# Kernel tuning notes

Measured on AMD Instinct MI355X. Metric: run time of the kernel, lower is better.

Reference implementation:

```python
import jax, jax.numpy as jnp
import numpy as np

NUM_EMBEDDINGS = 1024
EMBEDDING_DIM = 64
COMMITMENT_COST = 0.25


def setup_inputs() -> dict:
    key = jax.random.key(0)
    k1, k2 = jax.random.split(key)
    inputs = jax.random.normal(k1, (2, 64, 32, 32, 32), dtype=jnp.float32)
    embedding = jax.random.normal(k2, (NUM_EMBEDDINGS, EMBEDDING_DIM), dtype=jnp.float32)
    return {"inputs": inputs, "embedding": embedding}


def reference(inputs, embedding):
    # inputs: [B, C, D, H, W], embedding: [K, C]
    B, C, D, H, W = inputs.shape
    # flatten_permutation = [0, 2, 3, 4, 1] -> [B*D*H*W, C]
    flat_input = jnp.transpose(inputs, (0, 2, 3, 4, 1)).reshape(-1, C)
    # squared euclidean distances [N, K]
    distances = (
        jnp.sum(flat_input**2, axis=1, keepdims=True)
        + jnp.sum(embedding**2, axis=1)[None, :]
        - 2.0 * flat_input @ embedding.T
    )
    # torch.max(-distances, dim=1)[1] == argmin of distances
    encoding_indices = jnp.argmax(-distances, axis=1)  # [N]
    encoding_indices_view = encoding_indices.reshape(B, D, H, W)
    # embed: lookup then quantization_permutation [0, 4, 1, 2, 3] -> channel-first
    quantized = embedding[encoding_indices_view]            # [B, D, H, W, C]
    quantized = jnp.transpose(quantized, (0, 4, 1, 2, 3))   # [B, C, D, H, W]
    # commitment loss: MSE(stop_grad(quantized), inputs)
    loss = COMMITMENT_COST * jnp.mean((jax.lax.stop_gradient(quantized) - inputs) ** 2)
    # straight-through estimator
    quantized_st = inputs + jax.lax.stop_gradient(quantized - inputs)
    # eval path: encodings_sum = zeros(256) (hardcoded in original forward)
    encodings_sum = jnp.zeros(256, dtype=jnp.float32)
    return quantized_st, loss, encoding_indices_view, encodings_sum, embedding
```

## Files before the change

### kernel.cpp

```cpp
#include <hip/hip_runtime.h>
#include <stdint.h>

#define KCODES  1024
#define CDIM    64
#define SPATIAL 32768
#define NPOS    65536
#define NEL     4194304

#define OUT_Q    0
#define OUT_LOSS 4194304
#define OUT_IDX  4194305
#define OUT_SUM  4259841
#define OUT_EMB  4260097

#define NSET  32
#define SETB  8192
#define EIOFF 262144
#define BPOS  256

typedef _Float16 half8  __attribute__((ext_vector_type(8)));
typedef float    f32x4  __attribute__((ext_vector_type(4)));
typedef float    f32x16 __attribute__((ext_vector_type(16)));

__global__ void prep_emb(const float* __restrict__ emb, char* __restrict__ ws,
                         float* __restrict__ out) {
    int gt = blockIdx.x * 256 + threadIdx.x;
    if (gt == 0) out[OUT_LOSS] = 0.f;
    if (gt < 256) out[OUT_SUM + gt] = 0.f;
    {
        float4 v = *(const float4*)(emb + (size_t)gt * 4);
        float* o = out + OUT_EMB + (size_t)gt * 4;
        o[0] = v.x; o[1] = v.y; o[2] = v.z; o[3] = v.w;
    }
    if (gt < 8192) {
        int k = gt >> 3, oct = gt & 7;
        int set = k >> 5, row = k & 31;
        int ks = oct >> 1, hc = oct & 1;
        const float* e = emb + (size_t)k * CDIM + oct * 8;
        char* rec = ws + (size_t)set * SETB;
        _Float16* hi = (_Float16*)(rec + (ks * 2 + 0) * 1024 + (hc * 32 + row) * 16);
        _Float16* lo = (_Float16*)(rec + (ks * 2 + 1) * 1024 + (hc * 32 + row) * 16);
        float s2 = 0.f;
        half8 hv, lv;
#pragma unroll
        for (int i = 0; i < 8; ++i) {
            float v = e[i];
            s2 = fmaf(v, v, s2);
            _Float16 h = (_Float16)v;
            hv[i] = h;
            lv[i] = (_Float16)(v - (float)h);
        }
        *(half8*)hi = hv;
        *(half8*)lo = lv;
        s2 += __shfl_xor(s2, 1);
        s2 += __shfl_xor(s2, 2);
        s2 += __shfl_xor(s2, 4);
        if (oct == 0) ((float*)(ws + EIOFF))[k] = -0.5f * s2;
    }
}

#define GLDS16(GSRC, LDST)                                                     \
    __builtin_amdgcn_global_load_lds(                                          \
        (const __attribute__((address_space(1))) void*)(GSRC),                 \
        (__attribute__((address_space(3))) void*)(LDST), 16, 0, 0)

__global__ __launch_bounds__(512, 2) void vq_kernel(
        const float* __restrict__ in, const float* __restrict__ emb,
        const char* __restrict__ wsA, float* __restrict__ out) {
    __shared__ __align__(16) char stg[2][SETB];
    __shared__ float xl[CDIM * 129];
    __shared__ int   kwin[BPOS];
    __shared__ float lred[8];

    const int tid  = threadIdx.x;
    const int lane = tid & 63, wv = tid >> 6;
    const int col  = lane & 31, h = lane >> 5;
    const int p0   = blockIdx.x * BPOS;
    const int b    = p0 >> 15;
    const int s0   = p0 & 32767;
    const float* xin = in + (size_t)b * (CDIM * SPATIAL) + s0;
    const float* eiG = (const float*)(wsA + EIOFF);

    GLDS16(wsA + (size_t)wv * 1024 + lane * 16, &stg[0][0] + wv * 1024 + lane * 16);

    half8 bh[4], bl[4];
    for (int H = 0; H < 2; ++H) {
        {
            int p = tid & 127, cq = tid >> 7;
#pragma unroll
            for (int j = 0; j < 16; ++j) {
                int c = cq * 16 + j;
                xl[c * 129 + p] = xin[(size_t)c * SPATIAL + H * 128 + p];
            }
        }
        __syncthreads();
        if ((wv >> 2) == H) {
            int pp = (wv & 3) * 32 + col;
#pragma unroll
            for (int ks = 0; ks < 4; ++ks)
#pragma unroll
                for (int j = 0; j < 8; ++j) {
                    int c = ks * 16 + h * 8 + j;
                    float v = xl[c * 129 + pp];
                    _Float16 hh = (_Float16)v;
                    bh[ks][j] = hh;
                    bl[ks][j] = (_Float16)(v - (float)hh);
                }
        }
        if (H == 0) {
            __syncthreads();
        } else {
            asm volatile("s_waitcnt vmcnt(0)" ::: "memory");
            __syncthreads();
        }
    }

    float best = -3.402823466e38f;
    int   bk   = 0;
#pragma unroll 2
    for (int it = 0; it < NSET; ++it) {
        char* cur = &stg[0][0] + (size_t)(it & 1) * SETB;
        if (it + 1 < NSET) {
            char* nxt = &stg[0][0] + (size_t)((it + 1) & 1) * SETB;
            GLDS16(wsA + (size_t)(it + 1) * SETB + wv * 1024 + lane * 16,
                   nxt + wv * 1024 + lane * 16);
        }
        f32x4 ei0 = *(const f32x4*)(eiG + it * 32 + 0 * 8 + 4 * h);
        f32x4 ei1 = *(const f32x4*)(eiG + it * 32 + 1 * 8 + 4 * h);
        f32x4 ei2 = *(const f32x4*)(eiG + it * 32 + 2 * 8 + 4 * h);
        f32x4 ei3 = *(const f32x4*)(eiG + it * 32 + 3 * 8 + 4 * h);

        f32x16 acc;
#pragma unroll
        for (int q = 0; q < 16; ++q) acc[q] = 0.f;
        const char* ap = cur + (size_t)lane * 16;
#pragma unroll
        for (int ks = 0; ks < 4; ++ks) {
            half8 ah = *(const half8*)(ap + (ks * 2 + 0) * 1024);
            half8 al = *(const half8*)(ap + (ks * 2 + 1) * 1024);
            acc = __builtin_amdgcn_mfma_f32_32x32x16_f16(ah, bh[ks], acc, 0, 0, 0);
            acc = __builtin_amdgcn_mfma_f32_32x32x16_f16(ah, bl[ks], acc, 0, 0, 0);
            acc = __builtin_amdgcn_mfma_f32_32x32x16_f16(al, bh[ks], acc, 0, 0, 0);
        }
        int kb = it * 32 + 4 * h;
#pragma unroll
        for (int m = 0; m < 4; ++m) {
            f32x4 ev = (m == 0) ? ei0 : (m == 1) ? ei1 : (m == 2) ? ei2 : ei3;
#pragma unroll
            for (int r = 0; r < 4; ++r) {
                float sc = acc[m * 4 + r] + ev[r];
                if (sc > best) { best = sc; bk = kb + m * 8 + r; }
            }
        }
        asm volatile("s_waitcnt vmcnt(0)" ::: "memory");
        __syncthreads();
    }

    {
        float os = __shfl_xor(best, 32);
        int   ok = __shfl_xor(bk, 32);
        if (os > best || (os == best && ok < bk)) { best = os; bk = ok; }
        if (lane < 32) {
            kwin[wv * 32 + col] = bk;
            out[OUT_IDX + p0 + wv * 32 + col] = (float)bk;
        }
    }
    __syncthreads();

    float lsum = 0.f;
    {
        int p = tid & 255, cq = tid >> 8;
        int kk = kwin[p];
        const float* eb = emb + (size_t)kk * CDIM;
        float* q = out + OUT_Q + (size_t)b * (CDIM * SPATIAL) + s0;
#pragma unroll
        for (int j = 0; j < 32; ++j) {
            int c = cq * 32 + j;
            float x = xin[(size_t)c * SPATIAL + p];
            float e = eb[c];
            float d = e - x;
            lsum = fmaf(d, d, lsum);
            q[(size_t)c * SPATIAL + p] = x + d;
        }
    }
#pragma unroll
    for (int off = 32; off > 0; off >>= 1) lsum += __shfl_down(lsum, off);
    if (lane == 0) lred[wv] = lsum;
    __syncthreads();
    if (tid == 0) {
        float t = 0.f;
#pragma unroll
        for (int w = 0; w < 8; ++w) t += lred[w];
        atomicAdd(out + OUT_LOSS, t * (0.25f / (float)NEL));
    }
}

extern "C" void kernel_launch(void* const* d_in, const int* in_sizes, int n_in,
                              void* d_out, int out_size, void* d_ws, size_t ws_size,
                              hipStream_t stream) {
    const float* in  = (const float*)d_in[0];
    const float* emb = (const float*)d_in[1];
    float* out = (float*)d_out;
    char*  ws  = (char*)d_ws;

    prep_emb<<<64, 256, 0, stream>>>(emb, ws, out);
    vq_kernel<<<NPOS / BPOS, 512, 0, stream>>>(in, emb, ws, out);
}
```

Before: 50.15 us.

## Split codebook across waves with register-held embedding slices and LDS argmin merge

Each block now handles 128 positions instead of 256. Each wave owns a subset of codebook sets across four passes, reading the codebook fragments straight from global memory into registers and reading the split fp16 input fragments from LDS. This replaces the double-buffered LDS codebook streaming and its per-iteration barrier. The -0.5|e|^2 bias is pre-laid out to match the accumulator layout and used as the MFMA initial accumulator, which removes the separate bias add. Per-wave candidates are merged through LDS, and a higher occupancy target lets more blocks fit per CU, at the cost of more LDS traffic for the input fragments and an extra merge stage.

```diff
diff --git a/kernel.cpp b/kernel.cpp
--- a/kernel.cpp
+++ b/kernel.cpp
@@ -15,8 +15,9 @@
 
 #define NSET  32
 #define SETB  8192
-#define EIOFF 262144
-#define BPOS  256
+#define EIEXP 262144
+#define BPOS  128
+#define NPASS 4
 
 typedef _Float16 half8  __attribute__((ext_vector_type(8)));
 typedef float    f32x4  __attribute__((ext_vector_type(4)));
@@ -55,20 +56,21 @@
         s2 += __shfl_xor(s2, 1);
         s2 += __shfl_xor(s2, 2);
         s2 += __shfl_xor(s2, 4);
-        if (oct == 0) ((float*)(ws + EIOFF))[k] = -0.5f * s2;
+        if (oct == 0) {
+            int hh = (row >> 2) & 1;
+            int q  = (row & 3) | ((row >> 3) << 2);
+            ((float*)(ws + EIEXP))[(set * 2 + hh) * 16 + q] = -0.5f * s2;
+        }
     }
 }
 
-#define GLDS16(GSRC, LDST)                                                     \
-    __builtin_amdgcn_global_load_lds(                                          \
-        (const __attribute__((address_space(1))) void*)(GSRC),                 \
-        (__attribute__((address_space(3))) void*)(LDST), 16, 0, 0)
-
-__global__ __launch_bounds__(512, 2) void vq_kernel(
+__global__ __launch_bounds__(512, 4) void vq_kernel(
         const float* __restrict__ in, const float* __restrict__ emb,
         const char* __restrict__ wsA, float* __restrict__ out) {
-    __shared__ __align__(16) char stg[2][SETB];
     __shared__ float xl[CDIM * 129];
+    __shared__ __align__(16) char bfr[4 * 4 * 2 * 1024];
+    __shared__ float candS[8][BPOS];
+    __shared__ int   candK[8][BPOS];
     __shared__ int   kwin[BPOS];
     __shared__ float lred[8];
 
@@ -79,103 +81,127 @@
     const int b    = p0 >> 15;
     const int s0   = p0 & 32767;
     const float* xin = in + (size_t)b * (CDIM * SPATIAL) + s0;
-    const float* eiG = (const float*)(wsA + EIOFF);
-
-    GLDS16(wsA + (size_t)wv * 1024 + lane * 16, &stg[0][0] + wv * 1024 + lane * 16);
-
-    half8 bh[4], bl[4];
-    for (int H = 0; H < 2; ++H) {
-        {
-            int p = tid & 127, cq = tid >> 7;
-#pragma unroll
-            for (int j = 0; j < 16; ++j) {
-                int c = cq * 16 + j;
-                xl[c * 129 + p] = xin[(size_t)c * SPATIAL + H * 128 + p];
+
+    {
+        int p = tid & 127, cq = tid >> 7;
+#pragma unroll
+        for (int j = 0; j < 16; ++j) {
+            int c = cq * 16 + j;
+            xl[c * 129 + p] = xin[(size_t)c * SPATIAL + p];
+        }
+    }
+#pragma unroll
+    for (int i = tid; i < 8 * BPOS; i += 512) {
+        candS[i >> 7][i & 127] = -3.402823466e38f;
+        candK[i >> 7][i & 127] = 0;
+    }
+    __syncthreads();
+
+#pragma unroll
+    for (int s = tid; s < 1024; s += 512) {
+        int t = s >> 8, ks = (s >> 6) & 3, l = s & 63;
+        int pos = t * 32 + (l & 31);
+        int c0  = ks * 16 + (l >> 5) * 8;
+        half8 hv, lv;
+#pragma unroll
+        for (int i = 0; i < 8; ++i) {
+            float v = xl[(c0 + i) * 129 + pos];
+            _Float16 hh = (_Float16)v;
+            hv[i] = hh;
+            lv[i] = (_Float16)(v - (float)hh);
+        }
+        *(half8*)(bfr + (size_t)((t * 4 + ks) * 2 + 0) * 1024 + l * 16) = hv;
+        *(half8*)(bfr + (size_t)((t * 4 + ks) * 2 + 1) * 1024 + l * 16) = lv;
+    }
+    __syncthreads();
+
+#pragma unroll 1
+    for (int pass = 0; pass < NPASS; ++pass) {
+        const int set = pass * 8 + wv;
+        const char* rec = wsA + (size_t)set * SETB;
+        const char* ap  = rec + (size_t)lane * 16;
+        half8 ah0 = *(const half8*)(ap);
+        half8 al0 = *(const half8*)(ap + 1024);
+        half8 ah1 = *(const half8*)(ap + 2048);
+        half8 al1 = *(const half8*)(ap + 3072);
+        half8 ah2 = *(const half8*)(ap + 4096);
+        half8 al2 = *(const half8*)(ap + 5120);
+        half8 ah3 = *(const half8*)(ap + 6144);
+        half8 al3 = *(const half8*)(ap + 7168);
+        f32x16 eiv = *(const f32x16*)((const float*)(wsA + EIEXP) + (set * 2 + h) * 16);
+        const int kbase = set * 32 + 4 * h;
+
+#pragma unroll
+        for (int t = 0; t < 4; ++t) {
+            const char* bp = bfr + (size_t)t * 8192 + (size_t)lane * 16;
+            half8 bh0 = *(const half8*)(bp);
+            half8 bl0 = *(const half8*)(bp + 1024);
+            half8 bh1 = *(const half8*)(bp + 2048);
+            half8 bl1 = *(const half8*)(bp + 3072);
+            half8 bh2 = *(const half8*)(bp + 4096);
+            half8 bl2 = *(const half8*)(bp + 5120);
+            half8 bh3 = *(const half8*)(bp + 6144);
+            half8 bl3 = *(const half8*)(bp + 7168);
+            f32x16 a;
+            a = __builtin_amdgcn_mfma_f32_32x32x16_f16(ah0, bh0, eiv, 0, 0, 0);
+            a = __builtin_amdgcn_mfma_f32_32x32x16_f16(ah0, bl0, a, 0, 0, 0);
+            a = __builtin_amdgcn_mfma_f32_32x32x16_f16(al0, bh0, a, 0, 0, 0);
+            a = __builtin_amdgcn_mfma_f32_32x32x16_f16(ah1, bh1, a, 0, 0, 0);
+            a = __builtin_amdgcn_mfma_f32_32x32x16_f16(ah1, bl1, a, 0, 0, 0);
+            a = __builtin_amdgcn_mfma_f32_32x32x16_f16(al1, bh1, a, 0, 0, 0);
+            a = __builtin_amdgcn_mfma_f32_32x32x16_f16(ah2, bh2, a, 0, 0, 0);
+            a = __builtin_amdgcn_mfma_f32_32x32x16_f16(ah2, bl2, a, 0, 0, 0);
+            a = __builtin_amdgcn_mfma_f32_32x32x16_f16(al2, bh2, a, 0, 0, 0);
+            a = __builtin_amdgcn_mfma_f32_32x32x16_f16(ah3, bh3, a, 0, 0, 0);
+            a = __builtin_amdgcn_mfma_f32_32x32x16_f16(ah3, bl3, a, 0, 0, 0);
+            a = __builtin_amdgcn_mfma_f32_32x32x16_f16(al3, bh3, a, 0, 0, 0);
+
+            float bs = a[0];
+            int   bk = kbase;
+#pragma unroll
+            for (int q = 1; q < 16; ++q) {
+                float sc = a[q];
+                int   kk = kbase + (q & 3) + 8 * (q >> 2);
+                if (sc > bs) { bs = sc; bk = kk; }
             }
-        }
-        __syncthreads();
-        if ((wv >> 2) == H) {
-            int pp = (wv & 3) * 32 + col;
-#pragma unroll
-            for (int ks = 0; ks < 4; ++ks)
-#pragma unroll
-                for (int j = 0; j < 8; ++j) {
-                    int c = ks * 16 + h * 8 + j;
-                    float v = xl[c * 129 + pp];
-                    _Float16 hh = (_Float16)v;
-                    bh[ks][j] = hh;
-                    bl[ks][j] = (_Float16)(v - (float)hh);
-                }
-        }
-        if (H == 0) {
-            __syncthreads();
-        } else {
-            asm volatile("s_waitcnt vmcnt(0)" ::: "memory");
-            __syncthreads();
-        }
-    }
-
-    float best = -3.402823466e38f;
-    int   bk   = 0;
-#pragma unroll 2
-    for (int it = 0; it < NSET; ++it) {
-        char* cur = &stg[0][0] + (size_t)(it & 1) * SETB;
-        if (it + 1 < NSET) {
-            char* nxt = &stg[0][0] + (size_t)((it + 1) & 1) * SETB;
-            GLDS16(wsA + (size_t)(it + 1) * SETB + wv * 1024 + lane * 16,
-                   nxt + wv * 1024 + lane * 16);
-        }
-        f32x4 ei0 = *(const f32x4*)(eiG + it * 32 + 0 * 8 + 4 * h);
-        f32x4 ei1 = *(const f32x4*)(eiG + it * 32 + 1 * 8 + 4 * h);
-        f32x4 ei2 = *(const f32x4*)(eiG + it * 32 + 2 * 8 + 4 * h);
-        f32x4 ei3 = *(const f32x4*)(eiG + it * 32 + 3 * 8 + 4 * h);
-
-        f32x16 acc;
-#pragma unroll
-        for (int q = 0; q < 16; ++q) acc[q] = 0.f;
-        const char* ap = cur + (size_t)lane * 16;
-#pragma unroll
-        for (int ks = 0; ks < 4; ++ks) {
-            half8 ah = *(const half8*)(ap + (ks * 2 + 0) * 1024);
-            half8 al = *(const half8*)(ap + (ks * 2 + 1) * 1024);
-            acc = __builtin_amdgcn_mfma_f32_32x32x16_f16(ah, bh[ks], acc, 0, 0, 0);
-            acc = __builtin_amdgcn_mfma_f32_32x32x16_f16(ah, bl[ks], acc, 0, 0, 0);
-            acc = __builtin_amdgcn_mfma_f32_32x32x16_f16(al, bh[ks], acc, 0, 0, 0);
-        }
-        int kb = it * 32 + 4 * h;
-#pragma unroll
-        for (int m = 0; m < 4; ++m) {
-            f32x4 ev = (m == 0) ? ei0 : (m == 1) ? ei1 : (m == 2) ? ei2 : ei3;
-#pragma unroll
-            for (int r = 0; r < 4; ++r) {
-                float sc = acc[m * 4 + r] + ev[r];
-                if (sc > best) { best = sc; bk = kb + m * 8 + r; }
+            {
+                float os = __shfl_xor(bs, 32);
+                int   ok = __shfl_xor(bk, 32);
+                if (os > bs || (os == bs && ok < bk)) { bs = os; bk = ok; }
             }
-        }
-        asm volatile("s_waitcnt vmcnt(0)" ::: "memory");
-        __syncthreads();
-    }
-
-    {
-        float os = __shfl_xor(best, 32);
-        int   ok = __shfl_xor(bk, 32);
-        if (os > best || (os == best && ok < bk)) { best = os; bk = ok; }
-        if (lane < 32) {
-            kwin[wv * 32 + col] = bk;
-            out[OUT_IDX + p0 + wv * 32 + col] = (float)bk;
-        }
+            if (h == 0) {
+                int pc = t * 32 + col;
+                float cs = candS[wv][pc];
+                if (bs > cs) { candS[wv][pc] = bs; candK[wv][pc] = bk; }
+            }
+        }
+    }
+    __syncthreads();
+
+    if (tid < BPOS) {
+        int p = tid;
+        float bs = candS[0][p];
+        int   bk = candK[0][p];
+#pragma unroll
+        for (int w = 1; w < 8; ++w) {
+            float sc = candS[w][p];
+            int   kk = candK[w][p];
+            if (sc > bs || (sc == bs && kk < bk)) { bs = sc; bk = kk; }
+        }
+        kwin[p] = bk;
+        out[OUT_IDX + p0 + p] = (float)bk;
     }
     __syncthreads();
 
     float lsum = 0.f;
     {
-        int p = tid & 255, cq = tid >> 8;
+        int p = tid & 127, cq = tid >> 7;
         int kk = kwin[p];
         const float* eb = emb + (size_t)kk * CDIM;
         float* q = out + OUT_Q + (size_t)b * (CDIM * SPATIAL) + s0;
 #pragma unroll
-        for (int j = 0; j < 32; ++j) {
-            int c = cq * 32 + j;
+        for (int j = 0; j < 16; ++j) {
+            int c = cq * 16 + j;
             float x = xin[(size_t)c * SPATIAL + p];
             float e = eb[c];
             float d = e - x;
```

After: 99.35 us. 98.1% more time.

## Triple-buffer codebook staging and split MFMA accumulators to break dependency chain

Applied to the files above, without the earlier changes.

Switches codebook staging from a double to a triple LDS buffer with prefetch two sets ahead and vmcnt(1) waits, so each iteration has a single barrier. The -0.5*||e||^2 bias is stored in MFMA output order, preloaded into LDS, and used as the initial accumulator. The three MFMA chains (hi*hi, hi*lo, lo*hi) now go to independent accumulators so they can issue back-to-back, and the three results are summed once per set. This costs more LDS and registers, which may lower occupancy, and the changed summation order can move tie-break behaviour slightly.

```diff
diff --git a/kernel.cpp b/kernel.cpp
--- a/kernel.cpp
+++ b/kernel.cpp
@@ -15,7 +15,7 @@
 
 #define NSET  32
 #define SETB  8192
-#define EIOFF 262144
+#define EIEXP 262144
 #define BPOS  256
 
 typedef _Float16 half8  __attribute__((ext_vector_type(8)));
@@ -55,7 +55,11 @@
         s2 += __shfl_xor(s2, 1);
         s2 += __shfl_xor(s2, 2);
         s2 += __shfl_xor(s2, 4);
-        if (oct == 0) ((float*)(ws + EIOFF))[k] = -0.5f * s2;
+        if (oct == 0) {
+            int hh = (row >> 2) & 1;
+            int q  = (row & 3) | ((row >> 3) << 2);
+            ((float*)(ws + EIEXP))[(set * 2 + hh) * 16 + q] = -0.5f * s2;
+        }
     }
 }
 
@@ -67,8 +71,9 @@
 __global__ __launch_bounds__(512, 2) void vq_kernel(
         const float* __restrict__ in, const float* __restrict__ emb,
         const char* __restrict__ wsA, float* __restrict__ out) {
-    __shared__ __align__(16) char stg[2][SETB];
+    __shared__ __align__(16) char stg[3][SETB];
     __shared__ float xl[CDIM * 129];
+    __shared__ __align__(16) float eiL[NSET * 32];
     __shared__ int   kwin[BPOS];
     __shared__ float lred[8];
 
@@ -79,9 +84,10 @@
     const int b    = p0 >> 15;
     const int s0   = p0 & 32767;
     const float* xin = in + (size_t)b * (CDIM * SPATIAL) + s0;
-    const float* eiG = (const float*)(wsA + EIOFF);
-
-    GLDS16(wsA + (size_t)wv * 1024 + lane * 16, &stg[0][0] + wv * 1024 + lane * 16);
+    const float* eiG = (const float*)(wsA + EIEXP);
+
+    eiL[tid] = eiG[tid];
+    eiL[tid + 512] = eiG[tid + 512];
 
     half8 bh[4], bl[4];
     for (int H = 0; H < 2; ++H) {
@@ -107,53 +113,47 @@
                     bl[ks][j] = (_Float16)(v - (float)hh);
                 }
         }
-        if (H == 0) {
-            __syncthreads();
-        } else {
-            asm volatile("s_waitcnt vmcnt(0)" ::: "memory");
-            __syncthreads();
-        }
-    }
+        __syncthreads();
+    }
+
+    GLDS16(wsA + 0 * SETB + wv * 1024 + lane * 16, &stg[0][0] + wv * 1024 + lane * 16);
+    GLDS16(wsA + 1 * SETB + wv * 1024 + lane * 16, &stg[1][0] + wv * 1024 + lane * 16);
 
     float best = -3.402823466e38f;
     int   bk   = 0;
-#pragma unroll 2
+    char* cur = &stg[0][0];
+    char* nxt = &stg[1][0];
+    char* fut = &stg[2][0];
+#pragma unroll 1
     for (int it = 0; it < NSET; ++it) {
-        char* cur = &stg[0][0] + (size_t)(it & 1) * SETB;
-        if (it + 1 < NSET) {
-            char* nxt = &stg[0][0] + (size_t)((it + 1) & 1) * SETB;
-            GLDS16(wsA + (size_t)(it + 1) * SETB + wv * 1024 + lane * 16,
-                   nxt + wv * 1024 + lane * 16);
-        }
-        f32x4 ei0 = *(const f32x4*)(eiG + it * 32 + 0 * 8 + 4 * h);
-        f32x4 ei1 = *(const f32x4*)(eiG + it * 32 + 1 * 8 + 4 * h);
-        f32x4 ei2 = *(const f32x4*)(eiG + it * 32 + 2 * 8 + 4 * h);
-        f32x4 ei3 = *(const f32x4*)(eiG + it * 32 + 3 * 8 + 4 * h);
-
-        f32x16 acc;
-#pragma unroll
-        for (int q = 0; q < 16; ++q) acc[q] = 0.f;
+        asm volatile("s_waitcnt vmcnt(1)" ::: "memory");
+        __syncthreads();
+        {
+            int sN = (it + 2) & (NSET - 1);
+            GLDS16(wsA + (size_t)sN * SETB + wv * 1024 + lane * 16,
+                   fut + wv * 1024 + lane * 16);
+        }
+        f32x16 aA = *(const f32x16*)&eiL[(it * 2 + h) * 16];
+        f32x16 aB, aC;
+#pragma unroll
+        for (int q = 0; q < 16; ++q) { aB[q] = 0.f; aC[q] = 0.f; }
         const char* ap = cur + (size_t)lane * 16;
 #pragma unroll
         for (int ks = 0; ks < 4; ++ks) {
             half8 ah = *(const half8*)(ap + (ks * 2 + 0) * 1024);
             half8 al = *(const half8*)(ap + (ks * 2 + 1) * 1024);
-            acc = __builtin_amdgcn_mfma_f32_32x32x16_f16(ah, bh[ks], acc, 0, 0, 0);
-            acc = __builtin_amdgcn_mfma_f32_32x32x16_f16(ah, bl[ks], acc, 0, 0, 0);
-            acc = __builtin_amdgcn_mfma_f32_32x32x16_f16(al, bh[ks], acc, 0, 0, 0);
-        }
-        int kb = it * 32 + 4 * h;
-#pragma unroll
-        for (int m = 0; m < 4; ++m) {
-            f32x4 ev = (m == 0) ? ei0 : (m == 1) ? ei1 : (m == 2) ? ei2 : ei3;
-#pragma unroll
-            for (int r = 0; r < 4; ++r) {
-                float sc = acc[m * 4 + r] + ev[r];
-                if (sc > best) { best = sc; bk = kb + m * 8 + r; }
-            }
-        }
-        asm volatile("s_waitcnt vmcnt(0)" ::: "memory");
-        __syncthreads();
+            aA = __builtin_amdgcn_mfma_f32_32x32x16_f16(ah, bh[ks], aA, 0, 0, 0);
+            aB = __builtin_amdgcn_mfma_f32_32x32x16_f16(ah, bl[ks], aB, 0, 0, 0);
+            aC = __builtin_amdgcn_mfma_f32_32x32x16_f16(al, bh[ks], aC, 0, 0, 0);
+        }
+        const int kbase = it * 32 + 4 * h;
+#pragma unroll
+        for (int q = 0; q < 16; ++q) {
+            float sc = (aA[q] + aB[q]) + aC[q];
+            int   kk = kbase + (q & 3) + 8 * (q >> 2);
+            if (sc > best) { best = sc; bk = kk; }
+        }
+        char* t0 = cur; cur = nxt; nxt = fut; fut = t0;
     }
 
     {
```

New measurement: 49.04 us. 1.02x faster.

## Switch to 16x16 MFMA with per-wave codebook split and ring staging

Applied to the files above, without the earlier changes.

Rewrites the distance search to use 16x16x32 MFMAs. The block now covers 128 positions, and the two wave halves each scan half of the 1024 codes. Each wave streams its own codebook slices into a private double-buffered LDS ring, which removes the per-iteration block-wide barrier. The bias term is preloaded into the accumulator from a shared table. The argmax tracks only the winning set per row and defers index reconstruction to the end. Halving positions per block doubles the grid and the number of codebook reads, and a cross-half candidate merge is added through LDS.

```diff
diff --git a/kernel.cpp b/kernel.cpp
--- a/kernel.cpp
+++ b/kernel.cpp
@@ -13,14 +13,13 @@
 #define OUT_SUM  4259841
 #define OUT_EMB  4260097
 
-#define NSET  32
-#define SETB  8192
-#define EIOFF 262144
-#define BPOS  256
-
-typedef _Float16 half8  __attribute__((ext_vector_type(8)));
-typedef float    f32x4  __attribute__((ext_vector_type(4)));
-typedef float    f32x16 __attribute__((ext_vector_type(16)));
+#define NSET16 64
+#define SETB   4096
+#define EIOFF  262144
+#define BPOS   128
+
+typedef _Float16 half8 __attribute__((ext_vector_type(8)));
+typedef float    f32x4 __attribute__((ext_vector_type(4)));
 
 __global__ void prep_emb(const float* __restrict__ emb, char* __restrict__ ws,
                          float* __restrict__ out) {
@@ -34,12 +33,12 @@
     }
     if (gt < 8192) {
         int k = gt >> 3, oct = gt & 7;
-        int set = k >> 5, row = k & 31;
-        int ks = oct >> 1, hc = oct & 1;
+        int set = k >> 4, row = k & 15;
+        int s = oct >> 2, g = oct & 3;
         const float* e = emb + (size_t)k * CDIM + oct * 8;
         char* rec = ws + (size_t)set * SETB;
-        _Float16* hi = (_Float16*)(rec + (ks * 2 + 0) * 1024 + (hc * 32 + row) * 16);
-        _Float16* lo = (_Float16*)(rec + (ks * 2 + 1) * 1024 + (hc * 32 + row) * 16);
+        _Float16* hi = (_Float16*)(rec + s * 1024 + ((g << 4) | row) * 16);
+        _Float16* lo = (_Float16*)(rec + 2048 + s * 1024 + ((g << 4) | row) * 16);
         float s2 = 0.f;
         half8 hv, lv;
 #pragma unroll
@@ -67,115 +66,147 @@
 __global__ __launch_bounds__(512, 2) void vq_kernel(
         const float* __restrict__ in, const float* __restrict__ emb,
         const char* __restrict__ wsA, float* __restrict__ out) {
-    __shared__ __align__(16) char stg[2][SETB];
-    __shared__ float xl[CDIM * 129];
+    __shared__ __align__(16) char ring[8][2][SETB];
+    __shared__ __align__(16) float eiL[KCODES];
+    __shared__ float candS[2][BPOS];
+    __shared__ int   candK[2][BPOS];
     __shared__ int   kwin[BPOS];
     __shared__ float lred[8];
 
     const int tid  = threadIdx.x;
     const int lane = tid & 63, wv = tid >> 6;
-    const int col  = lane & 31, h = lane >> 5;
+    const int col  = lane & 15, g = lane >> 4;
+    const int pg   = wv & 3, kh = wv >> 2;
     const int p0   = blockIdx.x * BPOS;
     const int b    = p0 >> 15;
     const int s0   = p0 & 32767;
     const float* xin = in + (size_t)b * (CDIM * SPATIAL) + s0;
-    const float* eiG = (const float*)(wsA + EIOFF);
-
-    GLDS16(wsA + (size_t)wv * 1024 + lane * 16, &stg[0][0] + wv * 1024 + lane * 16);
-
-    half8 bh[4], bl[4];
-    for (int H = 0; H < 2; ++H) {
-        {
-            int p = tid & 127, cq = tid >> 7;
-#pragma unroll
-            for (int j = 0; j < 16; ++j) {
-                int c = cq * 16 + j;
-                xl[c * 129 + p] = xin[(size_t)c * SPATIAL + H * 128 + p];
+
+    float* xl = (float*)&ring[0][0][0];
+    {
+        int p = tid & 127, cq = tid >> 7;
+#pragma unroll
+        for (int j = 0; j < 16; ++j) {
+            int c = cq * 16 + j;
+            xl[c * 129 + p] = xin[(size_t)c * SPATIAL + p];
+        }
+    }
+    eiL[tid]       = ((const float*)(wsA + EIOFF))[tid];
+    eiL[tid + 512] = ((const float*)(wsA + EIOFF))[tid + 512];
+    __syncthreads();
+
+    half8 bh[2][2], bl[2][2];
+#pragma unroll
+    for (int nt = 0; nt < 2; ++nt)
+#pragma unroll
+        for (int s = 0; s < 2; ++s) {
+            int pp = pg * 32 + nt * 16 + col;
+#pragma unroll
+            for (int j = 0; j < 8; ++j) {
+                int c = s * 32 + g * 8 + j;
+                float v = xl[c * 129 + pp];
+                _Float16 hh = (_Float16)v;
+                bh[nt][s][j] = hh;
+                bl[nt][s][j] = (_Float16)(v - (float)hh);
             }
         }
-        __syncthreads();
-        if ((wv >> 2) == H) {
-            int pp = (wv & 3) * 32 + col;
-#pragma unroll
-            for (int ks = 0; ks < 4; ++ks)
-#pragma unroll
-                for (int j = 0; j < 8; ++j) {
-                    int c = ks * 16 + h * 8 + j;
-                    float v = xl[c * 129 + pp];
-                    _Float16 hh = (_Float16)v;
-                    bh[ks][j] = hh;
-                    bl[ks][j] = (_Float16)(v - (float)hh);
-                }
-        }
-        if (H == 0) {
-            __syncthreads();
-        } else {
-            asm volatile("s_waitcnt vmcnt(0)" ::: "memory");
-            __syncthreads();
-        }
-    }
-
-    float best = -3.402823466e38f;
-    int   bk   = 0;
-#pragma unroll 2
-    for (int it = 0; it < NSET; ++it) {
-        char* cur = &stg[0][0] + (size_t)(it & 1) * SETB;
-        if (it + 1 < NSET) {
-            char* nxt = &stg[0][0] + (size_t)((it + 1) & 1) * SETB;
-            GLDS16(wsA + (size_t)(it + 1) * SETB + wv * 1024 + lane * 16,
-                   nxt + wv * 1024 + lane * 16);
-        }
-        f32x4 ei0 = *(const f32x4*)(eiG + it * 32 + 0 * 8 + 4 * h);
-        f32x4 ei1 = *(const f32x4*)(eiG + it * 32 + 1 * 8 + 4 * h);
-        f32x4 ei2 = *(const f32x4*)(eiG + it * 32 + 2 * 8 + 4 * h);
-        f32x4 ei3 = *(const f32x4*)(eiG + it * 32 + 3 * 8 + 4 * h);
-
-        f32x16 acc;
-#pragma unroll
-        for (int q = 0; q < 16; ++q) acc[q] = 0.f;
-        const char* ap = cur + (size_t)lane * 16;
-#pragma unroll
-        for (int ks = 0; ks < 4; ++ks) {
-            half8 ah = *(const half8*)(ap + (ks * 2 + 0) * 1024);
-            half8 al = *(const half8*)(ap + (ks * 2 + 1) * 1024);
-            acc = __builtin_amdgcn_mfma_f32_32x32x16_f16(ah, bh[ks], acc, 0, 0, 0);
-            acc = __builtin_amdgcn_mfma_f32_32x32x16_f16(ah, bl[ks], acc, 0, 0, 0);
-            acc = __builtin_amdgcn_mfma_f32_32x32x16_f16(al, bh[ks], acc, 0, 0, 0);
-        }
-        int kb = it * 32 + 4 * h;
-#pragma unroll
-        for (int m = 0; m < 4; ++m) {
-            f32x4 ev = (m == 0) ? ei0 : (m == 1) ? ei1 : (m == 2) ? ei2 : ei3;
-#pragma unroll
-            for (int r = 0; r < 4; ++r) {
-                float sc = acc[m * 4 + r] + ev[r];
-                if (sc > best) { best = sc; bk = kb + m * 8 + r; }
-            }
-        }
-        asm volatile("s_waitcnt vmcnt(0)" ::: "memory");
-        __syncthreads();
-    }
-
-    {
-        float os = __shfl_xor(best, 32);
-        int   ok = __shfl_xor(bk, 32);
-        if (os > best || (os == best && ok < bk)) { best = os; bk = ok; }
-        if (lane < 32) {
-            kwin[wv * 32 + col] = bk;
-            out[OUT_IDX + p0 + wv * 32 + col] = (float)bk;
-        }
+    __syncthreads();
+
+    const char* myws = wsA + (size_t)kh * 32 * SETB;
+    char* slotA = &ring[wv][0][0];
+    char* slotB = &ring[wv][1][0];
+#define STAGE4(RSET, DST) do {                                                 \
+        const char* s_ = myws + (size_t)(RSET) * SETB + lane * 16;             \
+        char* d_ = (DST) + lane * 16;                                          \
+        GLDS16(s_,        d_);                                                 \
+        GLDS16(s_ + 1024, d_ + 1024);                                          \
+        GLDS16(s_ + 2048, d_ + 2048);                                          \
+        GLDS16(s_ + 3072, d_ + 3072);                                          \
+    } while (0)
+    STAGE4(0, slotA);
+
+    f32x4 maxS0, maxS1;
+    int   maxR0[4], maxR1[4];
+#pragma unroll
+    for (int r = 0; r < 4; ++r) {
+        maxS0[r] = -3.402823466e38f; maxS1[r] = -3.402823466e38f;
+        maxR0[r] = 0;                maxR1[r] = 0;
+    }
+
+#pragma unroll 1
+    for (int r = 0; r < 32; ++r) {
+        STAGE4((r + 1) & 31, slotB);
+        const int set = kh * 32 + r;
+        asm volatile("s_waitcnt vmcnt(4)" ::: "memory");
+        f32x4 eiv = *(const f32x4*)&eiL[set * 16 + g * 4];
+        const char* ap = slotA + (size_t)lane * 16;
+        half8 ah0 = *(const half8*)(ap);
+        half8 ah1 = *(const half8*)(ap + 1024);
+        half8 al0 = *(const half8*)(ap + 2048);
+        half8 al1 = *(const half8*)(ap + 3072);
+        f32x4 a0 = __builtin_amdgcn_mfma_f32_16x16x32_f16(ah0, bh[0][0], eiv, 0, 0, 0);
+        f32x4 a1 = __builtin_amdgcn_mfma_f32_16x16x32_f16(ah0, bh[1][0], eiv, 0, 0, 0);
+        a0 = __builtin_amdgcn_mfma_f32_16x16x32_f16(ah1, bh[0][1], a0, 0, 0, 0);
+        a1 = __builtin_amdgcn_mfma_f32_16x16x32_f16(ah1, bh[1][1], a1, 0, 0, 0);
+        a0 = __builtin_amdgcn_mfma_f32_16x16x32_f16(ah0, bl[0][0], a0, 0, 0, 0);
+        a1 = __builtin_amdgcn_mfma_f32_16x16x32_f16(ah0, bl[1][0], a1, 0, 0, 0);
+        a0 = __builtin_amdgcn_mfma_f32_16x16x32_f16(ah1, bl[0][1], a0, 0, 0, 0);
+        a1 = __builtin_amdgcn_mfma_f32_16x16x32_f16(ah1, bl[1][1], a1, 0, 0, 0);
+        a0 = __builtin_amdgcn_mfma_f32_16x16x32_f16(al0, bh[0][0], a0, 0, 0, 0);
+        a1 = __builtin_amdgcn_mfma_f32_16x16x32_f16(al0, bh[1][0], a1, 0, 0, 0);
+        a0 = __builtin_amdgcn_mfma_f32_16x16x32_f16(al1, bh[0][1], a0, 0, 0, 0);
+        a1 = __builtin_amdgcn_mfma_f32_16x16x32_f16(al1, bh[1][1], a1, 0, 0, 0);
+#pragma unroll
+        for (int rr = 0; rr < 4; ++rr) {
+            if (a0[rr] > maxS0[rr]) { maxS0[rr] = a0[rr]; maxR0[rr] = set; }
+            if (a1[rr] > maxS1[rr]) { maxS1[rr] = a1[rr]; maxR1[rr] = set; }
+        }
+        char* t_ = slotA; slotA = slotB; slotB = t_;
+    }
+#undef STAGE4
+
+#pragma unroll
+    for (int nt = 0; nt < 2; ++nt) {
+        float bs = nt ? maxS1[0] : maxS0[0];
+        int   bk = (nt ? maxR1[0] : maxR0[0]) * 16 + g * 4;
+#pragma unroll
+        for (int rr = 1; rr < 4; ++rr) {
+            float sc = nt ? maxS1[rr] : maxS0[rr];
+            int   kk = (nt ? maxR1[rr] : maxR0[rr]) * 16 + g * 4 + rr;
+            if (sc > bs || (sc == bs && kk < bk)) { bs = sc; bk = kk; }
+        }
+#pragma unroll
+        for (int m = 16; m <= 32; m <<= 1) {
+            float os = __shfl_xor(bs, m);
+            int   ok = __shfl_xor(bk, m);
+            if (os > bs || (os == bs && ok < bk)) { bs = os; bk = ok; }
+        }
+        if (g == 0) {
+            candS[kh][pg * 32 + nt * 16 + col] = bs;
+            candK[kh][pg * 32 + nt * 16 + col] = bk;
+        }
+    }
+    __syncthreads();
+
+    if (tid < BPOS) {
+        float s0v = candS[0][tid], s1v = candS[1][tid];
+        int   k0v = candK[0][tid], k1v = candK[1][tid];
+        int sel = (s1v > s0v) || (s1v == s0v && k1v < k0v);
+        int bkf = sel ? k1v : k0v;
+        kwin[tid] = bkf;
+        out[OUT_IDX + p0 + tid] = (float)bkf;
     }
     __syncthreads();
 
     float lsum = 0.f;
     {
-        int p = tid & 255, cq = tid >> 8;
+        int p = tid & 127, cq = tid >> 7;
         int kk = kwin[p];
         const float* eb = emb + (size_t)kk * CDIM;
         float* q = out + OUT_Q + (size_t)b * (CDIM * SPATIAL) + s0;
 #pragma unroll
-        for (int j = 0; j < 32; ++j) {
-            int c = cq * 32 + j;
+        for (int j = 0; j < 16; ++j) {
+            int c = cq * 16 + j;
             float x = xin[(size_t)c * SPATIAL + p];
             float e = eb[c];
             float d = e - x;
```

Result: faster. 44.93 us (-10.4%).
